# Optimization experiments

Hardware: AMD Instinct MI355X
Metric: run time of the kernel (lower is better)

The kernel has to match this reference:

```python
import jax, jax.numpy as jnp
import numpy as np

B, N, CT = 64, 256, 3
HID, HEADS = 256, 4
C = HID // HEADS          # per-head channels
E = 8192                  # number of edges
NEG = 0.2                 # GATv2 leaky_relu negative slope
EPS_BN = 1e-5


def setup_inputs() -> dict:
    key = jax.random.key(0)
    ks = jax.random.split(key, 32)
    F_in = N * CT
    s1 = 1.0 / np.sqrt(F_in)
    sh = 1.0 / np.sqrt(HID)
    inp = {
        "x": jax.random.normal(ks[0], (B, N, N, CT), jnp.float32),
        "edge_index": jax.random.randint(ks[1], (2, E), 0, N, dtype=jnp.int32),
        # node_proj: Linear + BatchNorm1d (eval) params
        "W1": jax.random.normal(ks[2], (F_in, HID), jnp.float32) * s1,
        "b1": jnp.zeros((HID,), jnp.float32),
        "g1": jnp.ones((HID,), jnp.float32),
        "be1": jnp.zeros((HID,), jnp.float32),
        "m1": jnp.zeros((HID,), jnp.float32),
        "v1": jnp.ones((HID,), jnp.float32),
        # GATv2 layer 0
        "Wl0": jax.random.normal(ks[3], (HID, HID), jnp.float32) * sh,
        "bl0": jnp.zeros((HID,), jnp.float32),
        "Wr0": jax.random.normal(ks[4], (HID, HID), jnp.float32) * sh,
        "br0": jnp.zeros((HID,), jnp.float32),
        "att0": jax.random.normal(ks[5], (HEADS, C), jnp.float32) * (1.0 / np.sqrt(C)),
        "bo0": jnp.zeros((HID,), jnp.float32),
        # GATv2 layer 1
        "Wl1": jax.random.normal(ks[6], (HID, HID), jnp.float32) * sh,
        "bl1": jnp.zeros((HID,), jnp.float32),
        "Wr1": jax.random.normal(ks[7], (HID, HID), jnp.float32) * sh,
        "br1": jnp.zeros((HID,), jnp.float32),
        "att1": jax.random.normal(ks[8], (HEADS, C), jnp.float32) * (1.0 / np.sqrt(C)),
        "bo1": jnp.zeros((HID,), jnp.float32),
        # output_proj: Linear + BatchNorm1d (eval) params
        "W2": jax.random.normal(ks[9], (HID, HID), jnp.float32) * sh,
        "b2": jnp.zeros((HID,), jnp.float32),
        "g2": jnp.ones((HID,), jnp.float32),
        "be2": jnp.zeros((HID,), jnp.float32),
        "m2": jnp.zeros((HID,), jnp.float32),
        "v2": jnp.ones((HID,), jnp.float32),
    }
    return inp


def _bn(x, g, b, m, v):
    # BatchNorm1d in eval mode: per-feature affine with running stats
    return (x - m) * jax.lax.rsqrt(v + EPS_BN) * g + b


def _gatv2(h, src, dst, Wl, bl, Wr, br, att, bo):
    # h: (N, HID). GATv2Conv (PyG semantics): lin_l on source, lin_r on target.
    xl = (h @ Wl + bl).reshape(N, HEADS, C)
    xr = (h @ Wr + br).reshape(N, HEADS, C)
    x_j = xl[src]                        # (E, H, C) source features
    x_i = xr[dst]                        # (E, H, C) target features
    e = jax.nn.leaky_relu(x_i + x_j, NEG)
    logits = jnp.einsum('ehc,hc->eh', e, att)          # (E, H)
    mx = jax.ops.segment_max(logits, dst, num_segments=N)
    a = jnp.exp(logits - mx[dst])
    den = jax.ops.segment_sum(a, dst, num_segments=N)
    a = a / (den[dst] + 1e-16)                         # neighborhood softmax
    out = jax.ops.segment_sum(x_j * a[:, :, None], dst, num_segments=N)
    return out.reshape(N, HID) + bo


def reference(x, edge_index, W1, b1, g1, be1, m1, v1,
              Wl0, bl0, Wr0, br0, att0, bo0,
              Wl1, bl1, Wr1, br1, att1, bo1,
              W2, b2, g2, be2, m2, v2):
    gelu = lambda t: jax.nn.gelu(t, approximate=False)
    xf = x.reshape(B, N, N * CT)
    # node_proj (eval: dropout off, BN uses running stats -> vmappable)
    h = gelu(_bn(xf @ W1 + b1, g1, be1, m1, v1))       # (B, N, HID)
    src, dst = edge_index[0], edge_index[1]

    def per_sample(hn):
        h0 = gelu(_gatv2(hn, src, dst, Wl0, bl0, Wr0, br0, att0, bo0))
        h1 = gelu(_gatv2(h0, src, dst, Wl1, bl1, Wr1, br1, att1, bo1))
        return h1.mean(axis=0)                          # mean over nodes

    pooled = jax.vmap(per_sample)(h)                    # (B, HID)
    return gelu(_bn(pooled @ W2 + b2, g2, be2, m2, v2))
```

## Files before the change

kernel.cpp:

```cpp
#include <hip/hip_runtime.h>
#include <hip/hip_bf16.h>
#include <math.h>

#define BATCH   64
#define NNODES  256
#define HID     256
#define HEADS   4
#define CDIM    64
#define NEDGES  8192
#define NEG_SLOPE 0.2f
#define EPS_BN 1e-5f


typedef __bf16 bf16_t;
typedef __bf16 bf16x8 __attribute__((ext_vector_type(8)));
typedef float  f32x4  __attribute__((ext_vector_type(4)));

__device__ __forceinline__ float gelu_f(float x) {
    return 0.5f * x * (1.0f + erff(x * 0.70710678118654752440f));
}

#define SWZ(r, c) ((c) ^ ((r) & 3) ^ (((r) >> 2) & 3) ^ (((r) >> 4) & 3))

__global__ __launch_bounds__(256) void prep_kernel(
        const int* __restrict__ ei,
        const float* __restrict__ W1, const float* __restrict__ Wa,
        const float* __restrict__ Wb, const float* __restrict__ Wc,
        const float* __restrict__ Wd,
        int* __restrict__ noff, int* __restrict__ csrc,
        bf16_t* __restrict__ T1, bf16_t* __restrict__ Ta,
        bf16_t* __restrict__ Tb, bf16_t* __restrict__ Tc,
        bf16_t* __restrict__ Td) {
    const int bx = blockIdx.x;
    const int tid = threadIdx.x;
    if (bx == 448) {
        __shared__ int cnt[NNODES];
        __shared__ int sc[NNODES];
        cnt[tid] = 0;
        __syncthreads();
        for (int e = tid; e < NEDGES; e += 256) atomicAdd(&cnt[ei[NEDGES + e]], 1);
        __syncthreads();
        sc[tid] = cnt[tid];
        __syncthreads();
        #pragma unroll
        for (int ofs = 1; ofs < 256; ofs <<= 1) {
            const int t = (tid >= ofs) ? sc[tid - ofs] : 0;
            __syncthreads();
            sc[tid] += t;
            __syncthreads();
        }
        const int excl = sc[tid] - cnt[tid];
        noff[tid] = excl;
        if (tid == 255) noff[NNODES] = sc[255];
        cnt[tid] = excl;
        __syncthreads();
        for (int e = tid; e < NEDGES; e += 256) {
            int d = ei[NEDGES + e];
            int p = atomicAdd(&cnt[d], 1);
            csrc[p] = ei[e];
        }
        return;
    }
    __shared__ float tile[32][33];
    const float* in; bf16_t* out; int t;
    if (bx < 192) { in = W1; out = T1; t = bx; }
    else {
        int r = bx - 192, mid = r >> 6; t = r & 63;
        if (mid == 0) { in = Wa; out = Ta; }
        else if (mid == 1) { in = Wb; out = Tb; }
        else if (mid == 2) { in = Wc; out = Tc; }
        else { in = Wd; out = Td; }
    }
    const int kt = t >> 3, nt = t & 7;
    const int k0 = kt * 32, n0 = nt * 32;
    const int x = tid & 31, y = tid >> 5;
    #pragma unroll
    for (int j = 0; j < 4; ++j)
        tile[y + j * 8][x] = in[(size_t)(k0 + y + j * 8) * 256 + n0 + x];
    __syncthreads();
    #pragma unroll
    for (int j = 0; j < 4; ++j) {
        const int n = n0 + y + j * 8;
        out[((size_t)kt * 256 + n) * 32 + x] = (bf16_t)tile[x][y + j * 8];
    }
}

template<int A_F32, int DUAL, int EPI_BN, int PERM, int KTILES>
__global__ __launch_bounds__(256, 4) void gemm_kernel(
        const void* __restrict__ Ap,
        const bf16_t* __restrict__ Bt0, const bf16_t* __restrict__ Bt1,
        bf16_t* __restrict__ C0p, bf16_t* __restrict__ C1p,
        const float* __restrict__ bias0, const float* __restrict__ bias1,
        const float* __restrict__ g, const float* __restrict__ be,
        const float* __restrict__ mu, const float* __restrict__ var) {
    __shared__ bf16_t As[2][32 * 32];
    __shared__ bf16_t Bs[2][256 * 32];
    const int K = KTILES * 32;
    const int tid  = threadIdx.x;
    const int lane = tid & 63;
    const int wv   = tid >> 6;
    const int mblk = blockIdx.y * 32;
    const bool second = DUAL && (blockIdx.x == 1);
    const bf16_t* Bt = second ? Bt1 : Bt0;
    bf16_t* Cp = second ? C1p : C0p;
    const float* bias = second ? bias1 : bias0;

    f32x4 acc[2][4];
    #pragma unroll
    for (int f = 0; f < 2; ++f)
        #pragma unroll
        for (int t = 0; t < 4; ++t) acc[f][t] = (f32x4){0.f, 0.f, 0.f, 0.f};

    const int arow = (tid & 127) >> 2;
    const int achk = tid & 3;
    const int gr   = mblk + arow;
    const int arr  = PERM ? ((gr & 63) * 256 + (gr >> 6)) : gr;
    const int fm   = lane & 15, q = lane >> 4;
    const int bn   = tid >> 2;

    f32x4 a0, a1; bf16x8 aReg; bf16x8 bReg[4];

    if (tid < 128) {
        if (A_F32) {
            const float* ap = (const float*)Ap + (size_t)arr * K + achk * 8;
            a0 = *(const f32x4*)ap; a1 = *(const f32x4*)(ap + 4);
        } else {
            aReg = *(const bf16x8*)((const bf16_t*)Ap + (size_t)arr * K + achk * 8);
        }
    }
    {
        const bf16_t* panel = Bt + (size_t)tid * 8;
        #pragma unroll
        for (int c = 0; c < 4; ++c) bReg[c] = *(const bf16x8*)(panel + c * 2048);
    }

    #pragma unroll
    for (int kt = 0; kt < KTILES; ++kt) {
        const int buf = kt & 1;
        if (tid < 128) {
            bf16x8 v;
            if (A_F32) {
                #pragma unroll
                for (int j = 0; j < 4; ++j) { v[j] = (bf16_t)a0[j]; v[4 + j] = (bf16_t)a1[j]; }
            } else v = aReg;
            *(bf16x8*)(&As[buf][(arow * 4 + SWZ(arow, achk)) * 8]) = v;
        }
        #pragma unroll
        for (int c = 0; c < 4; ++c) {
            const int n = c * 64 + bn;
            *(bf16x8*)(&Bs[buf][(n * 4 + SWZ(n, achk)) * 8]) = bReg[c];
        }
        __syncthreads();
        if (kt + 1 < KTILES) {
            const int k0 = (kt + 1) * 32;
            if (tid < 128) {
                if (A_F32) {
                    const float* ap = (const float*)Ap + (size_t)arr * K + k0 + achk * 8;
                    a0 = *(const f32x4*)ap; a1 = *(const f32x4*)(ap + 4);
                } else {
                    aReg = *(const bf16x8*)((const bf16_t*)Ap + (size_t)arr * K + k0 + achk * 8);
                }
            }
            const bf16_t* panel = Bt + (size_t)(kt + 1) * (256 * 32) + (size_t)tid * 8;
            #pragma unroll
            for (int c = 0; c < 4; ++c) bReg[c] = *(const bf16x8*)(panel + c * 2048);
        }
        bf16x8 af[2], bfv[4];
        #pragma unroll
        for (int f = 0; f < 2; ++f) {
            const int r = f * 16 + fm;
            af[f] = *(const bf16x8*)(&As[buf][(r * 4 + SWZ(r, q)) * 8]);
        }
        #pragma unroll
        for (int t = 0; t < 4; ++t) {
            const int n = wv * 64 + t * 16 + fm;
            bfv[t] = *(const bf16x8*)(&Bs[buf][(n * 4 + SWZ(n, q)) * 8]);
        }
        #pragma unroll
        for (int f = 0; f < 2; ++f)
            #pragma unroll
            for (int t = 0; t < 4; ++t)
                acc[f][t] = __builtin_amdgcn_mfma_f32_16x16x32_bf16(
                    af[f], bfv[t], acc[f][t], 0, 0, 0);
    }

    const int quad = lane >> 4, cn = lane & 15;
    #pragma unroll
    for (int t = 0; t < 4; ++t) {
        const int n = wv * 64 + t * 16 + cn;
        const float bv = bias[n];
        float scale = 1.0f, shift = 0.0f;
        if (EPI_BN) {
            float s = g[n] * rsqrtf(var[n] + EPS_BN);
            scale = s;
            shift = be[n] - mu[n] * s;
        }
        #pragma unroll
        for (int f = 0; f < 2; ++f) {
            #pragma unroll
            for (int r = 0; r < 4; ++r) {
                const int m = mblk + f * 16 + quad * 4 + r;
                float val = acc[f][t][r] + bv;
                if (EPI_BN) val = gelu_f(val * scale + shift);
                Cp[(size_t)m * 256 + n] = (bf16_t)val;
            }
        }
    }
}

__global__ __launch_bounds__(256) void edge_kernel(
        const bf16_t* __restrict__ XL, const bf16_t* __restrict__ XR,
        const float* __restrict__ att, const float* __restrict__ bo,
        const int* __restrict__ noff, const int* __restrict__ csrc,
        bf16_t* __restrict__ Hout) {
    const int bid  = blockIdx.x;
    const int i    = bid >> 3;
    const int tid  = threadIdx.x;
    const int w    = tid >> 6;
    const int lane = tid & 63;
    const int bg   = lane >> 3;
    const int cg   = lane & 7;
    const int b    = (bid & 7) * 8 + bg;
    const int cbase = w * CDIM + cg * 8;
    const size_t orow = ((size_t)i * BATCH + b) * HID + cbase;
    const float* bor = bo + cbase;

    const int s0 = noff[i], s1 = noff[i + 1];
    if (s0 == s1) {
        bf16x8 ov;
        #pragma unroll
        for (int q = 0; q < 8; ++q) ov[q] = (bf16_t)gelu_f(bor[q]);
        *(bf16x8*)(Hout + orow) = ov;
        return;
    }

    float a6[8], a4[8], xi[8];
    {
        const float* ar = att + cbase;
        const bf16x8 xr = *(const bf16x8*)(XR + orow);
        #pragma unroll
        for (int q = 0; q < 8; ++q) {
            float a = ar[q];
            a6[q] = 0.6f * a; a4[q] = 0.4f * a;
            xi[q] = (float)xr[q];
        }
    }

    const bf16_t* XLb = XL + (size_t)b * HID + cbase;
    const size_t RSTR = (size_t)BATCH * HID;

    float mA = -1e30f, dA = 0.f, mB = -1e30f, dB = 0.f;
    float accA[8], accB[8];
    #pragma unroll
    for (int q = 0; q < 8; ++q) { accA[q] = 0.f; accB[q] = 0.f; }

    int jA = csrc[s0];
    int jB = csrc[(s0 + 1 < s1) ? s0 + 1 : s0];
    bf16x8 xA = *(const bf16x8*)(XLb + (size_t)jA * RSTR);
    bf16x8 xB = *(const bf16x8*)(XLb + (size_t)jB * RSTR);

    for (int e = s0; e < s1; e += 2) {
        const int nA = (e + 2 < s1) ? e + 2 : s0;
        const int nB = (e + 3 < s1) ? e + 3 : s0;
        const int jnA = csrc[nA], jnB = csrc[nB];
        const bf16x8 xnA = *(const bf16x8*)(XLb + (size_t)jnA * RSTR);
        const bf16x8 xnB = *(const bf16x8*)(XLb + (size_t)jnB * RSTR);

        float fA[8], fB[8];
        #pragma unroll
        for (int q = 0; q < 8; ++q) { fA[q] = (float)xA[q]; fB[q] = (float)xB[q]; }
        float pA = 0.f, pB = 0.f;
        #pragma unroll
        for (int q = 0; q < 8; ++q) {
            const float zA = xi[q] + fA[q];
            const float zB = xi[q] + fB[q];
            pA = fmaf(a6[q], zA, pA);
            pB = fmaf(a6[q], zB, pB);
            pA = fmaf(a4[q], __builtin_fabsf(zA), pA);
            pB = fmaf(a4[q], __builtin_fabsf(zB), pB);
        }
        pA += __shfl_xor(pA, 1, 64);  pB += __shfl_xor(pB, 1, 64);
        pA += __shfl_xor(pA, 2, 64);  pB += __shfl_xor(pB, 2, 64);
        pA += __shfl_xor(pA, 4, 64);  pB += __shfl_xor(pB, 4, 64);

        const float mnA = fmaxf(mA, pA);
        const float alA = __expf(mA - mnA);
        const float wA  = __expf(pA - mnA);
        const float vB  = (e + 1 < s1) ? 1.f : 0.f;
        const float mnB = fmaxf(mB, pB);
        const float alB = __expf(mB - mnB);
        const float wB  = __expf(pB - mnB) * vB;
        dA = dA * alA + wA;
        dB = dB * alB + wB;
        #pragma unroll
        for (int q = 0; q < 8; ++q) {
            accA[q] = fmaf(accA[q], alA, wA * fA[q]);
            accB[q] = fmaf(accB[q], alB, wB * fB[q]);
        }
        mA = mnA; mB = mnB;
        xA = xnA; xB = xnB;
    }

    const float mm = fmaxf(mA, mB);
    const float g1 = __expf(mA - mm);
    const float g2 = __expf(mB - mm);
    const float inv = 1.0f / (dA * g1 + dB * g2 + 1e-16f);
    bf16x8 ov;
    #pragma unroll
    for (int q = 0; q < 8; ++q) {
        const float o = (accA[q] * g1 + accB[q] * g2) * inv + bor[q];
        ov[q] = (bf16_t)gelu_f(o);
    }
    *(bf16x8*)(Hout + orow) = ov;
}

__global__ __launch_bounds__(256) void pool_kernel(const bf16_t* __restrict__ H1,
                                                   float* __restrict__ P) {
    const int b = blockIdx.x, c = blockIdx.y, f = threadIdx.x;
    const bf16_t* p = H1 + ((size_t)(c * 64) * BATCH + b) * HID + f;
    float s = 0.f;
    for (int n = 0; n < 64; ++n) s += (float)p[(size_t)n * BATCH * HID];
    P[((size_t)b * 4 + c) * HID + f] = s;
}

__global__ __launch_bounds__(256) void final_kernel(
        const float* __restrict__ P, const float* __restrict__ W2,
        const float* __restrict__ b2, const float* __restrict__ g2,
        const float* __restrict__ be2, const float* __restrict__ m2,
        const float* __restrict__ v2, float* __restrict__ out) {
    __shared__ float pl[HID];
    const int b = blockIdx.x, f = threadIdx.x;
    float s4 = 0.f;
    #pragma unroll
    for (int c = 0; c < 4; ++c) s4 += P[((size_t)b * 4 + c) * HID + f];
    pl[f] = s4 * (1.0f / (float)NNODES);
    __syncthreads();
    float s = 0.f;
    for (int k = 0; k < HID; ++k) s += pl[k] * W2[(size_t)k * HID + f];
    s += b2[f];
    const float scale = g2[f] * rsqrtf(v2[f] + EPS_BN);
    s = (s - m2[f]) * scale + be2[f];
    out[b * HID + f] = gelu_f(s);
}

extern "C" void kernel_launch(void* const* d_in, const int* in_sizes, int n_in,
                              void* d_out, int out_size, void* d_ws, size_t ws_size,
                              hipStream_t stream) {
    const float* x    = (const float*)d_in[0];
    const int*   ei   = (const int*)d_in[1];
    const float* W1   = (const float*)d_in[2];
    const float* b1   = (const float*)d_in[3];
    const float* g1   = (const float*)d_in[4];
    const float* be1  = (const float*)d_in[5];
    const float* m1   = (const float*)d_in[6];
    const float* v1   = (const float*)d_in[7];
    const float* Wl0  = (const float*)d_in[8];
    const float* bl0  = (const float*)d_in[9];
    const float* Wr0  = (const float*)d_in[10];
    const float* br0  = (const float*)d_in[11];
    const float* att0 = (const float*)d_in[12];
    const float* bo0  = (const float*)d_in[13];
    const float* Wl1  = (const float*)d_in[14];
    const float* bl1  = (const float*)d_in[15];
    const float* Wr1  = (const float*)d_in[16];
    const float* br1  = (const float*)d_in[17];
    const float* att1 = (const float*)d_in[18];
    const float* bo1  = (const float*)d_in[19];
    const float* W2   = (const float*)d_in[20];
    const float* b2   = (const float*)d_in[21];
    const float* g2   = (const float*)d_in[22];
    const float* be2  = (const float*)d_in[23];
    const float* m2   = (const float*)d_in[24];
    const float* v2   = (const float*)d_in[25];

    char* ws = (char*)d_ws;
    const int M = BATCH * NNODES;
    const size_t SZ_BF = (size_t)M * HID * sizeof(bf16_t);

    int*    noff = (int*)ws;                ws += 2048;
    int*    csrc = (int*)ws;                ws += 32768;
    bf16_t* W1t  = (bf16_t*)ws;             ws += 256 * 768 * 2;
    bf16_t* Wl0t = (bf16_t*)ws;             ws += 256 * 256 * 2;
    bf16_t* Wr0t = (bf16_t*)ws;             ws += 256 * 256 * 2;
    bf16_t* Wl1t = (bf16_t*)ws;             ws += 256 * 256 * 2;
    bf16_t* Wr1t = (bf16_t*)ws;             ws += 256 * 256 * 2;
    bf16_t* H    = (bf16_t*)ws;             ws += SZ_BF;
    bf16_t* H2   = (bf16_t*)ws;             ws += SZ_BF;
    bf16_t* XL   = (bf16_t*)ws;             ws += SZ_BF;
    bf16_t* XR   = (bf16_t*)ws;             ws += SZ_BF;
    float*  P    = (float*)ws;              ws += BATCH * 4 * HID * 4;

    prep_kernel<<<449, 256, 0, stream>>>(ei, W1, Wl0, Wr0, Wl1, Wr1,
                                         noff, csrc, W1t, Wl0t, Wr0t, Wl1t, Wr1t);

    gemm_kernel<1, 0, 1, 1, 24><<<dim3(1, 512), 256, 0, stream>>>(
        x, W1t, nullptr, H, nullptr, b1, nullptr, g1, be1, m1, v1);

    gemm_kernel<0, 1, 0, 0, 8><<<dim3(2, 512), 256, 0, stream>>>(
        H, Wl0t, Wr0t, XL, XR, bl0, br0, nullptr, nullptr, nullptr, nullptr);
    edge_kernel<<<NNODES * 8, 256, 0, stream>>>(XL, XR, att0, bo0, noff, csrc, H2);

    gemm_kernel<0, 1, 0, 0, 8><<<dim3(2, 512), 256, 0, stream>>>(
        H2, Wl1t, Wr1t, XL, XR, bl1, br1, nullptr, nullptr, nullptr, nullptr);
    edge_kernel<<<NNODES * 8, 256, 0, stream>>>(XL, XR, att1, bo1, noff, csrc, H);

    pool_kernel<<<dim3(BATCH, 4), 256, 0, stream>>>(H, P);
    final_kernel<<<BATCH, 256, 0, stream>>>(P, W2, b2, g2, be2, m2, v2,
                                            (float*)d_out);
}
```

Baseline: 278.8 us.

## Use fp32 FMA node projection, drop softmax max subtraction, fuse pool and final

The first node projection moves from a bf16 MFMA GEMM over a pre-transposed W1 to a scalar fp32 FMA kernel with register tiling, and the W1 transpose leaves the prep kernel. The edge softmax drops its running-max rescaling and exponentiates logits directly, which saves exp calls but can overflow for large logits. The separate pool and final kernels are merged into one kernel with 64 blocks that serially sum 256 nodes each. The GEMM template loses its unused fp32-A and BN-epilogue variants.

```diff
diff --git a/kernel.cpp b/kernel.cpp
--- a/kernel.cpp
+++ b/kernel.cpp
@@ -22,18 +22,103 @@
 
 #define SWZ(r, c) ((c) ^ ((r) & 3) ^ (((r) >> 2) & 3) ^ (((r) >> 4) & 3))
 
+__global__ __launch_bounds__(256, 4) void npv_kernel(
+        const float* __restrict__ x, const float* __restrict__ W1,
+        const float* __restrict__ b1, const float* __restrict__ g1,
+        const float* __restrict__ be1, const float* __restrict__ m1,
+        const float* __restrict__ v1, bf16_t* __restrict__ H) {
+    __shared__ float xs[32][33];
+    __shared__ float wsm[32][256];
+    const int tid = threadIdx.x;
+    const int mt  = tid & 7;
+    const int nt  = tid >> 3;
+    const int mblk = blockIdx.x * 32;
+
+    const int arow = tid >> 3;
+    const int akc  = (tid & 7) * 4;
+    const int gr   = mblk + arow;
+    const int arr  = (gr & 63) * 256 + (gr >> 6);
+    const float* xrow = x + (size_t)arr * 768;
+
+    float acc[4][8];
+    #pragma unroll
+    for (int r = 0; r < 4; ++r)
+        #pragma unroll
+        for (int c = 0; c < 8; ++c) acc[r][c] = 0.f;
+
+    f32x4 xv; f32x4 wv[8];
+    xv = *(const f32x4*)(xrow + akc);
+    #pragma unroll
+    for (int c = 0; c < 8; ++c) {
+        const int idx = c * 1024 + tid * 4;
+        wv[c] = *(const f32x4*)(W1 + (size_t)(idx >> 8) * 256 + (idx & 255));
+    }
+
+    for (int kt = 0; kt < 24; ++kt) {
+        #pragma unroll
+        for (int j = 0; j < 4; ++j) xs[akc + j][arow] = xv[j];
+        #pragma unroll
+        for (int c = 0; c < 8; ++c) {
+            const int idx = c * 1024 + tid * 4;
+            *(f32x4*)(&wsm[idx >> 8][idx & 255]) = wv[c];
+        }
+        __syncthreads();
+        if (kt + 1 < 24) {
+            const int k0 = (kt + 1) * 32;
+            xv = *(const f32x4*)(xrow + k0 + akc);
+            #pragma unroll
+            for (int c = 0; c < 8; ++c) {
+                const int idx = c * 1024 + tid * 4;
+                wv[c] = *(const f32x4*)(W1 + (size_t)(k0 + (idx >> 8)) * 256 + (idx & 255));
+            }
+        }
+        #pragma unroll 8
+        for (int kk = 0; kk < 32; ++kk) {
+            float xr[4];
+            #pragma unroll
+            for (int r = 0; r < 4; ++r) xr[r] = xs[kk][mt * 4 + r];
+            const f32x4 w0 = *(const f32x4*)(&wsm[kk][nt * 8]);
+            const f32x4 w1v = *(const f32x4*)(&wsm[kk][nt * 8 + 4]);
+            #pragma unroll
+            for (int r = 0; r < 4; ++r) {
+                #pragma unroll
+                for (int c = 0; c < 4; ++c) {
+                    acc[r][c]     = fmaf(xr[r], w0[c], acc[r][c]);
+                    acc[r][4 + c] = fmaf(xr[r], w1v[c], acc[r][4 + c]);
+                }
+            }
+        }
+        __syncthreads();
+    }
+
+    float scale[8], shift[8];
+    #pragma unroll
+    for (int c = 0; c < 8; ++c) {
+        const int n = nt * 8 + c;
+        const float s = g1[n] * rsqrtf(v1[n] + EPS_BN);
+        scale[c] = s;
+        shift[c] = (b1[n] - m1[n]) * s + be1[n];
+    }
+    #pragma unroll
+    for (int r = 0; r < 4; ++r) {
+        bf16x8 ov;
+        #pragma unroll
+        for (int c = 0; c < 8; ++c)
+            ov[c] = (bf16_t)gelu_f(acc[r][c] * scale[c] + shift[c]);
+        *(bf16x8*)(H + (size_t)(mblk + mt * 4 + r) * 256 + nt * 8) = ov;
+    }
+}
+
 __global__ __launch_bounds__(256) void prep_kernel(
         const int* __restrict__ ei,
-        const float* __restrict__ W1, const float* __restrict__ Wa,
-        const float* __restrict__ Wb, const float* __restrict__ Wc,
-        const float* __restrict__ Wd,
+        const float* __restrict__ Wa, const float* __restrict__ Wb,
+        const float* __restrict__ Wc, const float* __restrict__ Wd,
         int* __restrict__ noff, int* __restrict__ csrc,
-        bf16_t* __restrict__ T1, bf16_t* __restrict__ Ta,
-        bf16_t* __restrict__ Tb, bf16_t* __restrict__ Tc,
-        bf16_t* __restrict__ Td) {
+        bf16_t* __restrict__ Ta, bf16_t* __restrict__ Tb,
+        bf16_t* __restrict__ Tc, bf16_t* __restrict__ Td) {
     const int bx = blockIdx.x;
     const int tid = threadIdx.x;
-    if (bx == 448) {
+    if (bx == 256) {
         __shared__ int cnt[NNODES];
         __shared__ int sc[NNODES];
         cnt[tid] = 0;
@@ -62,15 +147,12 @@
         return;
     }
     __shared__ float tile[32][33];
-    const float* in; bf16_t* out; int t;
-    if (bx < 192) { in = W1; out = T1; t = bx; }
-    else {
-        int r = bx - 192, mid = r >> 6; t = r & 63;
-        if (mid == 0) { in = Wa; out = Ta; }
-        else if (mid == 1) { in = Wb; out = Tb; }
-        else if (mid == 2) { in = Wc; out = Tc; }
-        else { in = Wd; out = Td; }
-    }
+    const int mid = bx >> 6, t = bx & 63;
+    const float* in; bf16_t* out;
+    if (mid == 0) { in = Wa; out = Ta; }
+    else if (mid == 1) { in = Wb; out = Tb; }
+    else if (mid == 2) { in = Wc; out = Tc; }
+    else { in = Wd; out = Td; }
     const int kt = t >> 3, nt = t & 7;
     const int k0 = kt * 32, n0 = nt * 32;
     const int x = tid & 31, y = tid >> 5;
@@ -85,14 +167,12 @@
     }
 }
 
-template<int A_F32, int DUAL, int EPI_BN, int PERM, int KTILES>
+template<int KTILES>
 __global__ __launch_bounds__(256, 4) void gemm_kernel(
-        const void* __restrict__ Ap,
+        const bf16_t* __restrict__ Ap,
         const bf16_t* __restrict__ Bt0, const bf16_t* __restrict__ Bt1,
         bf16_t* __restrict__ C0p, bf16_t* __restrict__ C1p,
-        const float* __restrict__ bias0, const float* __restrict__ bias1,
-        const float* __restrict__ g, const float* __restrict__ be,
-        const float* __restrict__ mu, const float* __restrict__ var) {
+        const float* __restrict__ bias0, const float* __restrict__ bias1) {
     __shared__ bf16_t As[2][32 * 32];
     __shared__ bf16_t Bs[2][256 * 32];
     const int K = KTILES * 32;
@@ -100,7 +180,7 @@
     const int lane = tid & 63;
     const int wv   = tid >> 6;
     const int mblk = blockIdx.y * 32;
-    const bool second = DUAL && (blockIdx.x == 1);
+    const bool second = (blockIdx.x == 1);
     const bf16_t* Bt = second ? Bt1 : Bt0;
     bf16_t* Cp = second ? C1p : C0p;
     const float* bias = second ? bias1 : bias0;
@@ -113,21 +193,12 @@
 
     const int arow = (tid & 127) >> 2;
     const int achk = tid & 3;
-    const int gr   = mblk + arow;
-    const int arr  = PERM ? ((gr & 63) * 256 + (gr >> 6)) : gr;
     const int fm   = lane & 15, q = lane >> 4;
     const int bn   = tid >> 2;
 
-    f32x4 a0, a1; bf16x8 aReg; bf16x8 bReg[4];
-
-    if (tid < 128) {
-        if (A_F32) {
-            const float* ap = (const float*)Ap + (size_t)arr * K + achk * 8;
-            a0 = *(const f32x4*)ap; a1 = *(const f32x4*)(ap + 4);
-        } else {
-            aReg = *(const bf16x8*)((const bf16_t*)Ap + (size_t)arr * K + achk * 8);
-        }
-    }
+    bf16x8 aReg; bf16x8 bReg[4];
+    if (tid < 128)
+        aReg = *(const bf16x8*)(Ap + (size_t)(mblk + arow) * K + achk * 8);
     {
         const bf16_t* panel = Bt + (size_t)tid * 8;
         #pragma unroll
@@ -137,14 +208,8 @@
     #pragma unroll
     for (int kt = 0; kt < KTILES; ++kt) {
         const int buf = kt & 1;
-        if (tid < 128) {
-            bf16x8 v;
-            if (A_F32) {
-                #pragma unroll
-                for (int j = 0; j < 4; ++j) { v[j] = (bf16_t)a0[j]; v[4 + j] = (bf16_t)a1[j]; }
-            } else v = aReg;
-            *(bf16x8*)(&As[buf][(arow * 4 + SWZ(arow, achk)) * 8]) = v;
-        }
+        if (tid < 128)
+            *(bf16x8*)(&As[buf][(arow * 4 + SWZ(arow, achk)) * 8]) = aReg;
         #pragma unroll
         for (int c = 0; c < 4; ++c) {
             const int n = c * 64 + bn;
@@ -153,14 +218,8 @@
         __syncthreads();
         if (kt + 1 < KTILES) {
             const int k0 = (kt + 1) * 32;
-            if (tid < 128) {
-                if (A_F32) {
-                    const float* ap = (const float*)Ap + (size_t)arr * K + k0 + achk * 8;
-                    a0 = *(const f32x4*)ap; a1 = *(const f32x4*)(ap + 4);
-                } else {
-                    aReg = *(const bf16x8*)((const bf16_t*)Ap + (size_t)arr * K + k0 + achk * 8);
-                }
-            }
+            if (tid < 128)
+                aReg = *(const bf16x8*)(Ap + (size_t)(mblk + arow) * K + k0 + achk * 8);
             const bf16_t* panel = Bt + (size_t)(kt + 1) * (256 * 32) + (size_t)tid * 8;
             #pragma unroll
             for (int c = 0; c < 4; ++c) bReg[c] = *(const bf16x8*)(panel + c * 2048);
@@ -189,20 +248,12 @@
     for (int t = 0; t < 4; ++t) {
         const int n = wv * 64 + t * 16 + cn;
         const float bv = bias[n];
-        float scale = 1.0f, shift = 0.0f;
-        if (EPI_BN) {
-            float s = g[n] * rsqrtf(var[n] + EPS_BN);
-            scale = s;
-            shift = be[n] - mu[n] * s;
-        }
         #pragma unroll
         for (int f = 0; f < 2; ++f) {
             #pragma unroll
             for (int r = 0; r < 4; ++r) {
                 const int m = mblk + f * 16 + quad * 4 + r;
-                float val = acc[f][t][r] + bv;
-                if (EPI_BN) val = gelu_f(val * scale + shift);
-                Cp[(size_t)m * 256 + n] = (bf16_t)val;
+                Cp[(size_t)m * 256 + n] = (bf16_t)(acc[f][t][r] + bv);
             }
         }
     }
@@ -249,7 +300,7 @@
     const bf16_t* XLb = XL + (size_t)b * HID + cbase;
     const size_t RSTR = (size_t)BATCH * HID;
 
-    float mA = -1e30f, dA = 0.f, mB = -1e30f, dB = 0.f;
+    float dA = 0.f, dB = 0.f;
     float accA[8], accB[8];
     #pragma unroll
     for (int q = 0; q < 8; ++q) { accA[q] = 0.f; accB[q] = 0.f; }
@@ -283,64 +334,45 @@
         pA += __shfl_xor(pA, 2, 64);  pB += __shfl_xor(pB, 2, 64);
         pA += __shfl_xor(pA, 4, 64);  pB += __shfl_xor(pB, 4, 64);
 
-        const float mnA = fmaxf(mA, pA);
-        const float alA = __expf(mA - mnA);
-        const float wA  = __expf(pA - mnA);
-        const float vB  = (e + 1 < s1) ? 1.f : 0.f;
-        const float mnB = fmaxf(mB, pB);
-        const float alB = __expf(mB - mnB);
-        const float wB  = __expf(pB - mnB) * vB;
-        dA = dA * alA + wA;
-        dB = dB * alB + wB;
+        const float wA = __expf(pA);
+        const float wB = ((e + 1 < s1) ? 1.f : 0.f) * __expf(pB);
+        dA += wA; dB += wB;
         #pragma unroll
         for (int q = 0; q < 8; ++q) {
-            accA[q] = fmaf(accA[q], alA, wA * fA[q]);
-            accB[q] = fmaf(accB[q], alB, wB * fB[q]);
-        }
-        mA = mnA; mB = mnB;
+            accA[q] = fmaf(wA, fA[q], accA[q]);
+            accB[q] = fmaf(wB, fB[q], accB[q]);
+        }
         xA = xnA; xB = xnB;
     }
 
-    const float mm = fmaxf(mA, mB);
-    const float g1 = __expf(mA - mm);
-    const float g2 = __expf(mB - mm);
-    const float inv = 1.0f / (dA * g1 + dB * g2 + 1e-16f);
+    const float inv = 1.0f / (dA + dB + 1e-16f);
     bf16x8 ov;
     #pragma unroll
     for (int q = 0; q < 8; ++q) {
-        const float o = (accA[q] * g1 + accB[q] * g2) * inv + bor[q];
+        const float o = (accA[q] + accB[q]) * inv + bor[q];
         ov[q] = (bf16_t)gelu_f(o);
     }
     *(bf16x8*)(Hout + orow) = ov;
 }
 
-__global__ __launch_bounds__(256) void pool_kernel(const bf16_t* __restrict__ H1,
-                                                   float* __restrict__ P) {
-    const int b = blockIdx.x, c = blockIdx.y, f = threadIdx.x;
-    const bf16_t* p = H1 + ((size_t)(c * 64) * BATCH + b) * HID + f;
-    float s = 0.f;
-    for (int n = 0; n < 64; ++n) s += (float)p[(size_t)n * BATCH * HID];
-    P[((size_t)b * 4 + c) * HID + f] = s;
-}
-
-__global__ __launch_bounds__(256) void final_kernel(
-        const float* __restrict__ P, const float* __restrict__ W2,
+__global__ __launch_bounds__(256) void pf_kernel(
+        const bf16_t* __restrict__ H1, const float* __restrict__ W2,
         const float* __restrict__ b2, const float* __restrict__ g2,
         const float* __restrict__ be2, const float* __restrict__ m2,
         const float* __restrict__ v2, float* __restrict__ out) {
     __shared__ float pl[HID];
     const int b = blockIdx.x, f = threadIdx.x;
-    float s4 = 0.f;
-    #pragma unroll
-    for (int c = 0; c < 4; ++c) s4 += P[((size_t)b * 4 + c) * HID + f];
-    pl[f] = s4 * (1.0f / (float)NNODES);
+    float s = 0.f;
+    for (int n = 0; n < NNODES; ++n)
+        s += (float)H1[((size_t)n * BATCH + b) * HID + f];
+    pl[f] = s * (1.0f / (float)NNODES);
     __syncthreads();
-    float s = 0.f;
-    for (int k = 0; k < HID; ++k) s += pl[k] * W2[(size_t)k * HID + f];
-    s += b2[f];
+    float acc = 0.f;
+    for (int k = 0; k < HID; ++k) acc += pl[k] * W2[(size_t)k * HID + f];
+    acc += b2[f];
     const float scale = g2[f] * rsqrtf(v2[f] + EPS_BN);
-    s = (s - m2[f]) * scale + be2[f];
-    out[b * HID + f] = gelu_f(s);
+    acc = (acc - m2[f]) * scale + be2[f];
+    out[b * HID + f] = gelu_f(acc);
 }
 
 extern "C" void kernel_launch(void* const* d_in, const int* in_sizes, int n_in,
@@ -379,7 +411,6 @@
 
     int*    noff = (int*)ws;                ws += 2048;
     int*    csrc = (int*)ws;                ws += 32768;
-    bf16_t* W1t  = (bf16_t*)ws;             ws += 256 * 768 * 2;
     bf16_t* Wl0t = (bf16_t*)ws;             ws += 256 * 256 * 2;
     bf16_t* Wr0t = (bf16_t*)ws;             ws += 256 * 256 * 2;
     bf16_t* Wl1t = (bf16_t*)ws;             ws += 256 * 256 * 2;
@@ -388,23 +419,19 @@
     bf16_t* H2   = (bf16_t*)ws;             ws += SZ_BF;
     bf16_t* XL   = (bf16_t*)ws;             ws += SZ_BF;
     bf16_t* XR   = (bf16_t*)ws;             ws += SZ_BF;
-    float*  P    = (float*)ws;              ws += BATCH * 4 * HID * 4;
-
-    prep_kernel<<<449, 256, 0, stream>>>(ei, W1, Wl0, Wr0, Wl1, Wr1,
-                                         noff, csrc, W1t, Wl0t, Wr0t, Wl1t, Wr1t);
-
-    gemm_kernel<1, 0, 1, 1, 24><<<dim3(1, 512), 256, 0, stream>>>(
-        x, W1t, nullptr, H, nullptr, b1, nullptr, g1, be1, m1, v1);
-
-    gemm_kernel<0, 1, 0, 0, 8><<<dim3(2, 512), 256, 0, stream>>>(
-        H, Wl0t, Wr0t, XL, XR, bl0, br0, nullptr, nullptr, nullptr, nullptr);
+
+    npv_kernel<<<512, 256, 0, stream>>>(x, W1, b1, g1, be1, m1, v1, H);
+
+    prep_kernel<<<257, 256, 0, stream>>>(ei, Wl0, Wr0, Wl1, Wr1,
+                                         noff, csrc, Wl0t, Wr0t, Wl1t, Wr1t);
+
+    gemm_kernel<8><<<dim3(2, 512), 256, 0, stream>>>(
+        H, Wl0t, Wr0t, XL, XR, bl0, br0);
     edge_kernel<<<NNODES * 8, 256, 0, stream>>>(XL, XR, att0, bo0, noff, csrc, H2);
 
-    gemm_kernel<0, 1, 0, 0, 8><<<dim3(2, 512), 256, 0, stream>>>(
-        H2, Wl1t, Wr1t, XL, XR, bl1, br1, nullptr, nullptr, nullptr, nullptr);
+    gemm_kernel<8><<<dim3(2, 512), 256, 0, stream>>>(
+        H2, Wl1t, Wr1t, XL, XR, bl1, br1);
     edge_kernel<<<NNODES * 8, 256, 0, stream>>>(XL, XR, att1, bo1, noff, csrc, H);
 
-    pool_kernel<<<dim3(BATCH, 4), 256, 0, stream>>>(H, P);
-    final_kernel<<<BATCH, 256, 0, stream>>>(P, W2, b2, g2, be2, m2, v2,
-                                            (float*)d_out);
-}
+    pf_kernel<<<BATCH, 256, 0, stream>>>(H, W2, b2, g2, be2, m2, v2, (float*)d_out);
+}
```

Measured after the change: 340.7 us. +22.2%, slower.
